# Kernel tuning notes

Measured on AMD Instinct MI355X. Metric: run time of the kernel, lower is better.

## Reference

```python
import jax, jax.numpy as jnp
import numpy as np

B, S, E, H = 2, 2048, 1024, 16
DH = E // H  # 64
FF = 4 * E


def setup_inputs() -> dict:
    key = jax.random.key(0)
    ks = jax.random.split(key, 13)
    s = 0.02
    return {
        "x": jax.random.normal(ks[0], (B, S, E), dtype=jnp.float32),
        "Wq": jax.random.normal(ks[1], (H, E, DH), dtype=jnp.float32) * s,
        "Wk": jax.random.normal(ks[2], (H, E, DH), dtype=jnp.float32) * s,
        "Wv": jax.random.normal(ks[3], (H, E, DH), dtype=jnp.float32) * s,
        "Wo": jax.random.normal(ks[4], (E, E), dtype=jnp.float32) * s,
        "bo": jnp.zeros((E,), dtype=jnp.float32),
        "W1": jax.random.normal(ks[5], (E, FF), dtype=jnp.float32) * s,
        "b1": jnp.zeros((FF,), dtype=jnp.float32),
        "W2": jax.random.normal(ks[6], (FF, E), dtype=jnp.float32) * s,
        "b2": jnp.zeros((E,), dtype=jnp.float32),
        "g1": jnp.ones((E,), dtype=jnp.float32),
        "beta1": jnp.zeros((E,), dtype=jnp.float32),
        "g2": jnp.ones((E,), dtype=jnp.float32),
        "beta2": jnp.zeros((E,), dtype=jnp.float32),
    }


def _layernorm(x, g, b, eps=1e-5):
    mu = jnp.mean(x, axis=-1, keepdims=True)
    var = jnp.var(x, axis=-1, keepdims=True)
    return (x - mu) * jax.lax.rsqrt(var + eps) * g + b


def reference(x, Wq, Wk, Wv, Wo, bo, W1, b1, W2, b2, g1, beta1, g2, beta2):
    # Pre-LN attention (dropout is identity in eval mode)
    nx = _layernorm(x, g1, beta1)
    # per-head projections, batched over heads: [B,H,S,DH]
    q = jnp.einsum('bse,hed->bhsd', nx, Wq)
    k = jnp.einsum('bse,hed->bhsd', nx, Wk)
    v = jnp.einsum('bse,hed->bhsd', nx, Wv)
    scores = jnp.einsum('bhqd,bhkd->bhqk', q, k) * (DH ** -0.5)  # [B,H,S,S]
    seq = x.shape[1]
    causal = jnp.tril(jnp.ones((seq, seq), dtype=bool))
    scores = jnp.where(causal, scores, -jnp.inf)
    w = jax.nn.softmax(scores, axis=-1)
    attn = jnp.einsum('bhqk,bhkd->bhqd', w, v)  # [B,H,S,DH]
    # concat heads (head order matches ModuleList cat order)
    attn = attn.transpose(0, 2, 1, 3).reshape(x.shape[0], seq, E)
    attn_out = attn @ Wo + bo
    x = x + attn_out
    # FFN
    nx2 = _layernorm(x, g2, beta2)
    ffn = jax.nn.relu(nx2 @ W1 + b1) @ W2 + b2
    return x + ffn
```

## Files before the change

### kernel.cpp

```cpp
#include <hip/hip_runtime.h>


typedef __attribute__((ext_vector_type(8))) short short8;
typedef __attribute__((ext_vector_type(4))) float floatx4;

__device__ inline unsigned short f32_to_bf16(float f) {
  unsigned u = __float_as_uint(f);
  unsigned rb = (u >> 16) & 1u;
  u += 0x7fffu + rb;
  return (unsigned short)(u >> 16);
}
__device__ inline unsigned f32_to_bf16_hi(float f) {
  return (__float_as_uint(f) + 0x8000u) >> 16;
}
__device__ inline float bf16_to_f32(unsigned short u) {
  return __uint_as_float(((unsigned)u) << 16);
}

__device__ inline void gload16(const void* g, void* l) {
  __builtin_amdgcn_global_load_lds(
      (const __attribute__((address_space(1))) void*)g,
      (__attribute__((address_space(3))) void*)l, 16, 0, 0);
}

__global__ __launch_bounds__(256) void transpose_to_bf16(
    const float* __restrict__ in, unsigned short* __restrict__ out,
    int R, int C, int ldo, long in_bs, long out_bs) {
  __shared__ float tile[32][33];
  in  += (size_t)blockIdx.z * in_bs;
  out += (size_t)blockIdx.z * out_bs;
  const int c0 = blockIdx.x * 32, r0 = blockIdx.y * 32;
  const int tx = threadIdx.x & 31, ty = threadIdx.x >> 5;
#pragma unroll
  for (int i = 0; i < 32; i += 8)
    tile[ty + i][tx] = in[(size_t)(r0 + ty + i) * C + c0 + tx];
  __syncthreads();
#pragma unroll
  for (int i = 0; i < 32; i += 8)
    out[(size_t)(c0 + ty + i) * ldo + r0 + tx] = f32_to_bf16(tile[tx][ty + i]);
}

__global__ __launch_bounds__(256) void transpose_v(
    const unsigned short* __restrict__ qkv, unsigned short* __restrict__ vT) {
  __shared__ unsigned short tile[32][33];
  const int bh = blockIdx.z, b = bh >> 4, h = bh & 15;
  const int k0 = blockIdx.x * 32, d0 = blockIdx.y * 32;
  const int tx = threadIdx.x & 31, ty = threadIdx.x >> 5;
#pragma unroll
  for (int i = 0; i < 32; i += 8)
    tile[ty + i][tx] = qkv[(size_t)(b * 2048 + k0 + ty + i) * 3072 + 2048 + h * 64 + d0 + tx];
  __syncthreads();
#pragma unroll
  for (int i = 0; i < 32; i += 8)
    vT[((size_t)bh * 64 + d0 + ty + i) * 2048 + k0 + tx] = tile[tx][ty + i];
}

__global__ __launch_bounds__(256) void layernorm_bf16(
    const float* __restrict__ x, const float* __restrict__ g,
    const float* __restrict__ be, unsigned short* __restrict__ out) {
  const int row = blockIdx.x;
  const int t = threadIdx.x;
  floatx4 v = ((const floatx4*)(x + (size_t)row * 1024))[t];
  float s  = v[0] + v[1] + v[2] + v[3];
  float s2 = v[0]*v[0] + v[1]*v[1] + v[2]*v[2] + v[3]*v[3];
#pragma unroll
  for (int off = 1; off < 64; off <<= 1) {
    s  += __shfl_xor(s, off);
    s2 += __shfl_xor(s2, off);
  }
  __shared__ float red[8];
  const int wave = t >> 6, lane = t & 63;
  if (lane == 0) { red[wave] = s; red[wave + 4] = s2; }
  __syncthreads();
  float ts  = red[0] + red[1] + red[2] + red[3];
  float ts2 = red[4] + red[5] + red[6] + red[7];
  float mu  = ts * (1.f / 1024.f);
  float var = ts2 * (1.f / 1024.f) - mu * mu;
  float rs  = rsqrtf(var + 1e-5f);
  floatx4 gv = ((const floatx4*)g)[t];
  floatx4 bv = ((const floatx4*)be)[t];
  ushort4 ov;
  ov.x = f32_to_bf16((v[0] - mu) * rs * gv[0] + bv[0]);
  ov.y = f32_to_bf16((v[1] - mu) * rs * gv[1] + bv[1]);
  ov.z = f32_to_bf16((v[2] - mu) * rs * gv[2] + bv[2]);
  ov.w = f32_to_bf16((v[3] - mu) * rs * gv[3] + bv[3]);
  ((ushort4*)(out + (size_t)row * 1024))[t] = ov;
}

__global__ __launch_bounds__(256) void gemm_bf16(
    const unsigned short* __restrict__ A, const unsigned short* __restrict__ Bt,
    const float* __restrict__ bias, const float* __restrict__ resid,
    void* __restrict__ Cout, int M, int N, int Kfull, int Klen, int mode) {
  __shared__ unsigned short As[128 * 32];
  __shared__ unsigned short Bs[128 * 32];
  const int t = threadIdx.x;
  const int NB = gridDim.x;
  const int bid = blockIdx.y * NB + blockIdx.x;
  const int xcd = bid & 7, slot = bid >> 3;
  const int m0 = (xcd * 4 + slot / NB) * 128;
  const int n0 = (slot % NB) * 128;
  const int koff = blockIdx.z * Klen;
  const int lane = t & 63, wave = t >> 6;
  const int wm = (wave >> 1) * 64, wn = (wave & 1) * 64;
  const int l15 = lane & 15, quad = lane >> 4;

  floatx4 acc[4][4];
#pragma unroll
  for (int i = 0; i < 4; ++i)
#pragma unroll
    for (int j = 0; j < 4; ++j) acc[i][j] = floatx4{0.f, 0.f, 0.f, 0.f};

  const int srow = wave * 32 + (lane >> 2);
  const int scol = (lane & 3) * 8;
  const unsigned short* Ag0 = A + (size_t)(m0 + srow) * Kfull + koff + scol;
  const unsigned short* Ag1 = Ag0 + (size_t)16 * Kfull;
  const unsigned short* Bg0 = Bt + (size_t)(n0 + srow) * Kfull + koff + scol;
  const unsigned short* Bg1 = Bg0 + (size_t)16 * Kfull;
  unsigned short* lA0 = &As[(wave * 2 + 0) * 512];
  unsigned short* lA1 = &As[(wave * 2 + 1) * 512];
  unsigned short* lB0 = &Bs[(wave * 2 + 0) * 512];
  unsigned short* lB1 = &Bs[(wave * 2 + 1) * 512];

  const int KT = Klen >> 5;
  for (int kt = 0; kt < KT; ++kt) {
    const int ko = kt * 32;
    gload16(Ag0 + ko, lA0);
    gload16(Ag1 + ko, lA1);
    gload16(Bg0 + ko, lB0);
    gload16(Bg1 + ko, lB1);
    __syncthreads();
    short8 a[4], b[4];
#pragma unroll
    for (int i = 0; i < 4; ++i)
      a[i] = *(const short8*)&As[(wm + i * 16 + l15) * 32 + quad * 8];
#pragma unroll
    for (int i = 0; i < 4; ++i)
      b[i] = *(const short8*)&Bs[(wn + i * 16 + l15) * 32 + quad * 8];
#pragma unroll
    for (int i = 0; i < 4; ++i)
#pragma unroll
      for (int j = 0; j < 4; ++j)
        acc[i][j] = __builtin_amdgcn_mfma_f32_16x16x32_bf16(a[i], b[j], acc[i][j], 0, 0, 0);
    __syncthreads();
  }

  const size_t poff = (size_t)blockIdx.z * 4096 * 1024;
#pragma unroll
  for (int i = 0; i < 4; ++i)
#pragma unroll
    for (int j = 0; j < 4; ++j) {
      const int col = n0 + wn + j * 16 + l15;
      const int rb = m0 + wm + i * 16 + quad * 4;
#pragma unroll
      for (int r = 0; r < 4; ++r) {
        const int row = rb + r;
        float v = acc[i][j][r];
        if (mode == 0) {
          ((unsigned short*)Cout)[(size_t)row * N + col] = f32_to_bf16(v);
        } else if (mode == 1) {
          v += bias[col] + resid[(size_t)row * N + col];
          ((float*)Cout)[(size_t)row * N + col] = v;
        } else if (mode == 2) {
          v += bias[col];
          v = fmaxf(v, 0.f);
          ((unsigned short*)Cout)[(size_t)row * N + col] = f32_to_bf16(v);
        } else {
          ((float*)Cout)[poff + (size_t)row * N + col] = v;
        }
      }
    }
}

__global__ __launch_bounds__(256) void splitk_reduce(
    const float* __restrict__ p, const float* __restrict__ bias,
    const float* __restrict__ resid, float* __restrict__ out) {
  const int t = threadIdx.x;
  const size_t base = (size_t)blockIdx.x * 256 + t;
  floatx4 a = ((const floatx4*)p)[base];
  floatx4 b = ((const floatx4*)p)[1048576 + base];
  floatx4 rv = ((const floatx4*)resid)[base];
  floatx4 bv = ((const floatx4*)bias)[t];
  ((floatx4*)out)[base] = a + b + rv + bv;
}

__global__ __launch_bounds__(256) void splitk_reduce_ln(
    const float* __restrict__ p, const float* __restrict__ bias,
    const float* __restrict__ resid, const float* __restrict__ g,
    const float* __restrict__ be, float* __restrict__ xout,
    unsigned short* __restrict__ nxout) {
  const int row = blockIdx.x, t = threadIdx.x;
  const size_t base = (size_t)row * 256 + t;
  floatx4 a = ((const floatx4*)p)[base];
  floatx4 b = ((const floatx4*)p)[1048576 + base];
  floatx4 rv = ((const floatx4*)resid)[base];
  floatx4 bv = ((const floatx4*)bias)[t];
  floatx4 v = a + b + rv + bv;
  ((floatx4*)xout)[base] = v;
  float s  = v[0] + v[1] + v[2] + v[3];
  float s2 = v[0]*v[0] + v[1]*v[1] + v[2]*v[2] + v[3]*v[3];
#pragma unroll
  for (int off = 1; off < 64; off <<= 1) {
    s  += __shfl_xor(s, off);
    s2 += __shfl_xor(s2, off);
  }
  __shared__ float red[8];
  const int wave = t >> 6, lane = t & 63;
  if (lane == 0) { red[wave] = s; red[wave + 4] = s2; }
  __syncthreads();
  float ts  = red[0] + red[1] + red[2] + red[3];
  float ts2 = red[4] + red[5] + red[6] + red[7];
  float mu  = ts * (1.f / 1024.f);
  float var = ts2 * (1.f / 1024.f) - mu * mu;
  float rs  = rsqrtf(var + 1e-5f);
  floatx4 gv = ((const floatx4*)g)[t];
  floatx4 bev = ((const floatx4*)be)[t];
  ushort4 ov;
  ov.x = f32_to_bf16((v[0] - mu) * rs * gv[0] + bev[0]);
  ov.y = f32_to_bf16((v[1] - mu) * rs * gv[1] + bev[1]);
  ov.z = f32_to_bf16((v[2] - mu) * rs * gv[2] + bev[2]);
  ov.w = f32_to_bf16((v[3] - mu) * rs * gv[3] + bev[3]);
  ((ushort4*)(nxout + (size_t)row * 1024))[t] = ov;
}

__global__ __launch_bounds__(256, 3) void flash_attn_mfma(
    const unsigned short* __restrict__ qkv,
    const unsigned short* __restrict__ vT,
    unsigned short* __restrict__ attn) {
  const int b = blockIdx.z, h = blockIdx.y, bh = b * 16 + h;
  const int qt = 15 - (int)blockIdx.x;
  const int q0 = qt * 128;
  const int t = threadIdx.x;
  const int wave = t >> 6, lane = t & 63;
  const int l15 = lane & 15, quad = lane >> 4;

  __shared__ unsigned short Ks[2][64][68];
  __shared__ unsigned short Vs[2][64][68];
  __shared__ unsigned short Ps[4][32][68];

  const size_t qbase = (size_t)b * 2048 * 3072;
  const int qrow_w = q0 + wave * 32;
  const unsigned short* Kbase = qkv + qbase + 1024 + h * 64;
  const unsigned short* Vbase = vT + (size_t)bh * 64 * 2048;

  short8 qf[2][2];
#pragma unroll
  for (int mf = 0; mf < 2; ++mf)
#pragma unroll
    for (int kc = 0; kc < 2; ++kc) {
      short8 raw = *(const short8*)(qkv + qbase +
          (size_t)(qrow_w + mf * 16 + l15) * 3072 + h * 64 + kc * 32 + quad * 8);
      short8 sc;
#pragma unroll
      for (int j = 0; j < 8; ++j)
        sc[j] = (short)f32_to_bf16(bf16_to_f32((unsigned short)raw[j]) * 0.125f);
      qf[mf][kc] = sc;
    }

  floatx4 o[2][4];
  float l_s[2] = {0.f, 0.f};
#pragma unroll
  for (int mf = 0; mf < 2; ++mf)
#pragma unroll
    for (int jd = 0; jd < 4; ++jd) o[mf][jd] = floatx4{0.f, 0.f, 0.f, 0.f};

  const int sr = t >> 3, so = (t & 7) * 8;

  uint4 kr0 = *(const uint4*)(Kbase + (size_t)sr * 3072 + so);
  uint4 kr1 = *(const uint4*)(Kbase + (size_t)(sr + 32) * 3072 + so);
  uint4 vr0 = *(const uint4*)(Vbase + (size_t)sr * 2048 + so);
  uint4 vr1 = *(const uint4*)(Vbase + (size_t)(sr + 32) * 2048 + so);

  const int ntiles = 2 * qt + 2;
  int buf = 0;
  for (int kt = 0; kt < ntiles; ++kt) {
    const int k0 = kt * 64;
    *(uint4*)&Ks[buf][sr][so]      = kr0;
    *(uint4*)&Ks[buf][sr + 32][so] = kr1;
    *(uint4*)&Vs[buf][sr][so]      = vr0;
    *(uint4*)&Vs[buf][sr + 32][so] = vr1;
    if (kt + 1 < ntiles) {
      const int k1 = k0 + 64;
      kr0 = *(const uint4*)(Kbase + (size_t)(k1 + sr) * 3072 + so);
      kr1 = *(const uint4*)(Kbase + (size_t)(k1 + sr + 32) * 3072 + so);
      vr0 = *(const uint4*)(Vbase + (size_t)sr * 2048 + k1 + so);
      vr1 = *(const uint4*)(Vbase + (size_t)(sr + 32) * 2048 + k1 + so);
    }
    __syncthreads();

    if (k0 <= qrow_w + 31) {
      short8 kf[2][4];
#pragma unroll
      for (int kc = 0; kc < 2; ++kc)
#pragma unroll
        for (int jb = 0; jb < 4; ++jb)
          kf[kc][jb] = *(const short8*)&Ks[buf][jb * 16 + l15][kc * 32 + quad * 8];

      floatx4 st[2][4];
#pragma unroll
      for (int mf = 0; mf < 2; ++mf)
#pragma unroll
        for (int jb = 0; jb < 4; ++jb) st[mf][jb] = floatx4{0.f, 0.f, 0.f, 0.f};
#pragma unroll
      for (int kc = 0; kc < 2; ++kc)
#pragma unroll
        for (int jb = 0; jb < 4; ++jb) {
#pragma unroll
          for (int mf = 0; mf < 2; ++mf)
            st[mf][jb] = __builtin_amdgcn_mfma_f32_16x16x32_bf16(
                kf[kc][jb], qf[mf][kc], st[mf][jb], 0, 0, 0);
        }

#pragma unroll
      for (int mf = 0; mf < 2; ++mf) {
        const int qq = qrow_w + mf * 16 + l15;
#pragma unroll
        for (int jb = 0; jb < 4; ++jb) {
          const int keyb = k0 + jb * 16 + quad * 4;
          float p0 = (keyb + 0 > qq) ? 0.f : __expf(st[mf][jb][0]);
          float p1 = (keyb + 1 > qq) ? 0.f : __expf(st[mf][jb][1]);
          float p2 = (keyb + 2 > qq) ? 0.f : __expf(st[mf][jb][2]);
          float p3 = (keyb + 3 > qq) ? 0.f : __expf(st[mf][jb][3]);
          l_s[mf] += (p0 + p1) + (p2 + p3);
          uint2 pk;
          pk.x = (f32_to_bf16_hi(p1) << 16) | f32_to_bf16_hi(p0);
          pk.y = (f32_to_bf16_hi(p3) << 16) | f32_to_bf16_hi(p2);
          *(uint2*)&Ps[wave][mf * 16 + l15][jb * 16 + quad * 4] = pk;
        }
      }

#pragma unroll
      for (int kc = 0; kc < 2; ++kc) {
        short8 pf0 = *(const short8*)&Ps[wave][l15][kc * 32 + quad * 8];
        short8 pf1 = *(const short8*)&Ps[wave][16 + l15][kc * 32 + quad * 8];
#pragma unroll
        for (int jd = 0; jd < 4; ++jd) {
          short8 vf = *(const short8*)&Vs[buf][jd * 16 + l15][kc * 32 + quad * 8];
          o[0][jd] = __builtin_amdgcn_mfma_f32_16x16x32_bf16(pf0, vf, o[0][jd], 0, 0, 0);
          o[1][jd] = __builtin_amdgcn_mfma_f32_16x16x32_bf16(pf1, vf, o[1][jd], 0, 0, 0);
        }
      }
    }
    buf ^= 1;
  }

#pragma unroll
  for (int mf = 0; mf < 2; ++mf) {
    l_s[mf] += __shfl_xor(l_s[mf], 16);
    l_s[mf] += __shfl_xor(l_s[mf], 32);
  }

#pragma unroll
  for (int mf = 0; mf < 2; ++mf)
#pragma unroll
    for (int r = 0; r < 4; ++r) {
      const int qloc = quad * 4 + r;
      const float lsum = __shfl(l_s[mf], qloc);
      const float rl = 1.f / lsum;
      const int row = b * 2048 + q0 + wave * 32 + mf * 16 + qloc;
#pragma unroll
      for (int jd = 0; jd < 4; ++jd)
        attn[(size_t)row * 1024 + h * 64 + jd * 16 + l15] =
            f32_to_bf16(o[mf][jd][r] * rl);
    }
}

extern "C" void kernel_launch(void* const* d_in, const int* in_sizes, int n_in,
                              void* d_out, int out_size, void* d_ws, size_t ws_size,
                              hipStream_t stream) {
  const float* x   = (const float*)d_in[0];
  const float* Wq  = (const float*)d_in[1];
  const float* Wk  = (const float*)d_in[2];
  const float* Wv  = (const float*)d_in[3];
  const float* Wo  = (const float*)d_in[4];
  const float* bo  = (const float*)d_in[5];
  const float* W1  = (const float*)d_in[6];
  const float* b1  = (const float*)d_in[7];
  const float* W2  = (const float*)d_in[8];
  const float* b2  = (const float*)d_in[9];
  const float* g1  = (const float*)d_in[10];
  const float* be1 = (const float*)d_in[11];
  const float* g2  = (const float*)d_in[12];
  const float* be2 = (const float*)d_in[13];
  float* out = (float*)d_out;

  char* ws = (char*)d_ws;
  size_t off = 0;
  auto alloc = [&](size_t bytes) -> void* {
    void* p = ws + off;
    off += (bytes + 255) & ~(size_t)255;
    return p;
  };
  unsigned short* WqkvT = (unsigned short*)alloc(3072ull * 1024 * 2);
  unsigned short* WoT   = (unsigned short*)alloc(1024ull * 1024 * 2);
  unsigned short* W1T   = (unsigned short*)alloc(4096ull * 1024 * 2);
  unsigned short* W2T   = (unsigned short*)alloc(1024ull * 4096 * 2);
  unsigned short* nx    = (unsigned short*)alloc(4096ull * 1024 * 2);
  unsigned short* qkv   = (unsigned short*)alloc(4096ull * 3072 * 2);
  unsigned short* attn  = (unsigned short*)alloc(4096ull * 1024 * 2);
  float*          x1    = (float*)alloc(4096ull * 1024 * 4);
  unsigned short* nx2   = (unsigned short*)alloc(4096ull * 1024 * 2);
  unsigned short* hbuf  = (unsigned short*)alloc(4096ull * 4096 * 2);
  unsigned short* vT    = hbuf;
  float*          part  = (float*)nx;

  dim3 blk(256);
  transpose_to_bf16<<<dim3(2, 32, 16), blk, 0, stream>>>(Wq, WqkvT, 1024, 64, 1024, 65536, 65536);
  transpose_to_bf16<<<dim3(2, 32, 16), blk, 0, stream>>>(Wk, WqkvT + 1024 * 1024, 1024, 64, 1024, 65536, 65536);
  transpose_to_bf16<<<dim3(2, 32, 16), blk, 0, stream>>>(Wv, WqkvT + 2 * 1024 * 1024, 1024, 64, 1024, 65536, 65536);
  transpose_to_bf16<<<dim3(32, 32, 1), blk, 0, stream>>>(Wo, WoT, 1024, 1024, 1024, 0, 0);
  transpose_to_bf16<<<dim3(128, 32, 1), blk, 0, stream>>>(W1, W1T, 1024, 4096, 1024, 0, 0);
  transpose_to_bf16<<<dim3(32, 128, 1), blk, 0, stream>>>(W2, W2T, 4096, 1024, 4096, 0, 0);

  layernorm_bf16<<<4096, blk, 0, stream>>>(x, g1, be1, nx);
  gemm_bf16<<<dim3(24, 32, 1), blk, 0, stream>>>(nx, WqkvT, nullptr, nullptr, qkv, 4096, 3072, 1024, 1024, 0);
  transpose_v<<<dim3(64, 2, 32), blk, 0, stream>>>(qkv, vT);
  flash_attn_mfma<<<dim3(16, 16, 2), blk, 0, stream>>>(qkv, vT, attn);
  gemm_bf16<<<dim3(8, 32, 2), blk, 0, stream>>>(attn, WoT, nullptr, nullptr, part, 4096, 1024, 1024, 512, 3);
  splitk_reduce_ln<<<4096, blk, 0, stream>>>(part, bo, x, g2, be2, x1, nx2);
  gemm_bf16<<<dim3(32, 32, 1), blk, 0, stream>>>(nx2, W1T, b1, nullptr, hbuf, 4096, 4096, 1024, 1024, 2);
  gemm_bf16<<<dim3(8, 32, 2), blk, 0, stream>>>(hbuf, W2T, nullptr, nullptr, part, 4096, 1024, 4096, 2048, 3);
  splitk_reduce<<<4096, blk, 0, stream>>>(part, b2, x1, out);
}
```

Baseline: 425.1 us.

## Double-buffer GEMM LDS tiles to overlap global loads with MFMA

The bf16 GEMM now uses two LDS buffers per operand and prefetches the next K tile with global_load_lds while MFMAs run on the current one. It waits on the outstanding loads with an explicit vmcnt and raw s_barrier instead of __syncthreads. Launch bounds are set to request 4 blocks per CU. The goal is to hide global memory latency in the K loop, at the cost of twice the shared memory. The raw barrier does not wait on LDS (lgkmcnt), so there is some risk around ordering the LDS reads against the next overwrite.

```diff
diff --git a/kernel.cpp b/kernel.cpp
--- a/kernel.cpp
+++ b/kernel.cpp
@@ -87,12 +87,12 @@
   ((ushort4*)(out + (size_t)row * 1024))[t] = ov;
 }
 
-__global__ __launch_bounds__(256) void gemm_bf16(
+__global__ __launch_bounds__(256, 4) void gemm_bf16(
     const unsigned short* __restrict__ A, const unsigned short* __restrict__ Bt,
     const float* __restrict__ bias, const float* __restrict__ resid,
     void* __restrict__ Cout, int M, int N, int Kfull, int Klen, int mode) {
-  __shared__ unsigned short As[128 * 32];
-  __shared__ unsigned short Bs[128 * 32];
+  __shared__ unsigned short As[2][128 * 32];
+  __shared__ unsigned short Bs[2][128 * 32];
   const int t = threadIdx.x;
   const int NB = gridDim.x;
   const int bid = blockIdx.y * NB + blockIdx.x;
@@ -116,33 +116,44 @@
   const unsigned short* Ag1 = Ag0 + (size_t)16 * Kfull;
   const unsigned short* Bg0 = Bt + (size_t)(n0 + srow) * Kfull + koff + scol;
   const unsigned short* Bg1 = Bg0 + (size_t)16 * Kfull;
-  unsigned short* lA0 = &As[(wave * 2 + 0) * 512];
-  unsigned short* lA1 = &As[(wave * 2 + 1) * 512];
-  unsigned short* lB0 = &Bs[(wave * 2 + 0) * 512];
-  unsigned short* lB1 = &Bs[(wave * 2 + 1) * 512];
+  const int sbase0 = (wave * 2 + 0) * 512;
+  const int sbase1 = (wave * 2 + 1) * 512;
 
   const int KT = Klen >> 5;
+  gload16(Ag0, &As[0][sbase0]);
+  gload16(Ag1, &As[0][sbase1]);
+  gload16(Bg0, &Bs[0][sbase0]);
+  gload16(Bg1, &Bs[0][sbase1]);
+
+  int buf = 0;
   for (int kt = 0; kt < KT; ++kt) {
-    const int ko = kt * 32;
-    gload16(Ag0 + ko, lA0);
-    gload16(Ag1 + ko, lA1);
-    gload16(Bg0 + ko, lB0);
-    gload16(Bg1 + ko, lB1);
-    __syncthreads();
+    if (kt + 1 < KT) {
+      const int ko = (kt + 1) * 32;
+      gload16(Ag0 + ko, &As[buf ^ 1][sbase0]);
+      gload16(Ag1 + ko, &As[buf ^ 1][sbase1]);
+      gload16(Bg0 + ko, &Bs[buf ^ 1][sbase0]);
+      gload16(Bg1 + ko, &Bs[buf ^ 1][sbase1]);
+      asm volatile("s_waitcnt vmcnt(4)" ::: "memory");
+    } else {
+      asm volatile("s_waitcnt vmcnt(0)" ::: "memory");
+    }
+    __builtin_amdgcn_s_barrier();
     short8 a[4], b[4];
 #pragma unroll
     for (int i = 0; i < 4; ++i)
-      a[i] = *(const short8*)&As[(wm + i * 16 + l15) * 32 + quad * 8];
+      a[i] = *(const short8*)&As[buf][(wm + i * 16 + l15) * 32 + quad * 8];
 #pragma unroll
     for (int i = 0; i < 4; ++i)
-      b[i] = *(const short8*)&Bs[(wn + i * 16 + l15) * 32 + quad * 8];
+      b[i] = *(const short8*)&Bs[buf][(wn + i * 16 + l15) * 32 + quad * 8];
 #pragma unroll
     for (int i = 0; i < 4; ++i)
 #pragma unroll
       for (int j = 0; j < 4; ++j)
         acc[i][j] = __builtin_amdgcn_mfma_f32_16x16x32_bf16(a[i], b[j], acc[i][j], 0, 0, 0);
-    __syncthreads();
+    __builtin_amdgcn_s_barrier();
+    buf ^= 1;
   }
+  __builtin_amdgcn_sched_barrier(0);
 
   const size_t poff = (size_t)blockIdx.z * 4096 * 1024;
 #pragma unroll
```

After: 382.6 us. -10.0%, faster.
